# Kernel optimization log

Measured on AMD Instinct MI355X. Metric: run time of the kernel, lower is better.

## Reference

```python
import jax, jax.numpy as jnp
import numpy as np
import math

B, N, D = 16, 1024, 1024

def setup_inputs() -> dict:
    key = jax.random.key(0)
    k1, k2, k3, k4 = jax.random.split(key, 4)
    x = jax.random.normal(k1, (B, N, D), dtype=jnp.float32)
    # Keras 'random_normal' initializer defaults to stddev=0.05
    w_keys = jax.random.normal(k2, (N, N), dtype=jnp.float32) * 0.05
    w_queries = jax.random.normal(k3, (N, N), dtype=jnp.float32) * 0.05
    w_values = jax.random.normal(k4, (N, N), dtype=jnp.float32) * 0.05
    return {"x": x, "w_keys": w_keys, "w_queries": w_queries, "w_values": w_values}

def reference(x, w_keys, w_queries, w_values):
    # x: (B, N, D); weights: (N, N); fact = sqrt(N) per build(input_shape[1])
    fact = math.sqrt(x.shape[1])
    ip = jnp.swapaxes(x, 1, 2)              # (B, D, N)
    vk = ip @ w_keys                         # (B, D, N)
    vq = ip @ w_queries                      # (B, D, N)
    vv = ip @ w_values                       # (B, D, N)
    kq = jnp.einsum('bdn,ben->bde', vk, vq) / fact   # (B, D, D)
    sm = jax.nn.softmax(kq, axis=-1)         # softmax over last axis
    # tf: sm @ transpose(pm(vv)) == sm @ vv  since pm then transpose_b cancel
    out = jnp.einsum('bde,ben->bdn', sm, vv) # (B, D, N)
    return jnp.swapaxes(out, 1, 2)           # (B, N, D)
```

## Files before the change

kernel.cpp:

```cpp
#include <hip/hip_runtime.h>
#include <stdint.h>


typedef __bf16 bf16x8_t __attribute__((ext_vector_type(8)));
typedef float  f32x4_t  __attribute__((ext_vector_type(4)));

typedef __attribute__((address_space(3))) uint32_t as3_u32;
typedef __attribute__((address_space(1))) uint32_t as1_u32;

__device__ __forceinline__ void async_copy16(const void* g, const void* l) {
  __builtin_amdgcn_global_load_lds((const as1_u32*)(uintptr_t)g,
                                   (as3_u32*)(uint32_t)(uintptr_t)l,
                                   16, 0, 0);
}

__device__ __forceinline__ uint16_t f2bf(float f) {
  uint32_t x = __float_as_uint(f);
  return (uint16_t)((x + 0x7fffu + ((x >> 16) & 1u)) >> 16);
}
__device__ __forceinline__ float bf2f(uint16_t b) {
  return __uint_as_float(((uint32_t)b) << 16);
}

template <bool OUT_F32>
__global__ __launch_bounds__(512, 2)
void gemm_bt256(const uint16_t* __restrict__ A, const uint16_t* __restrict__ B,
                void* __restrict__ Cv, size_t sA, size_t sB, size_t sC,
                float alpha)
{
  __shared__ __align__(16) char smem[131072];

  const int lid  = blockIdx.x;
  const int xcd  = lid & 7;
  const int slot = lid >> 3;
  const int z    = (xcd << 1) | (slot >> 4);
  const int t16  = slot & 15;
  const int bm0  = (t16 >> 2) << 8;
  const int bn0  = (t16 & 3) << 8;

  A += (size_t)z * sA + ((size_t)bm0 << 10);
  B += (size_t)z * sB + ((size_t)bn0 << 10);

  const int t    = threadIdx.x;
  const int lane = t & 63;
  const int w    = t >> 6;
  const int q    = lane >> 4;
  const int r16  = lane & 15;
  const int wm   = (w >> 2) << 7;
  const int wn   = (w & 3) << 6;

  const int g0  = t >> 3;
  const int cp  = t & 7;
  const int ce  = (cp ^ (g0 & 7)) << 3;
  const int sAo = (g0 << 7) + (cp << 4);
  const int rB  = ((g0 >> 5) << 6) + (g0 & 31);
  const int sBo = (rB << 7) + (cp << 4);
  const uint16_t* Ab = A + ((size_t)g0 << 10) + ce;
  const uint16_t* Bb = B + ((size_t)rB << 10) + ce;

#define STAGE_A(s, kge, dst) do {                                              \
    async_copy16(Ab + (((s)*64 +   0) << 10) + (kge),                          \
                 smem + (dst) + sAo + (s)*8192);                               \
    async_copy16(Ab + (((s)*64 + 128) << 10) + (kge),                          \
                 smem + (dst) + sAo + (s)*8192 + 16384);                       \
  } while (0)
#define STAGE_B(s, kge, dst) do {                                              \
    async_copy16(Bb + (((s)*32 +   0) << 10) + (kge),                          \
                 smem + (dst) + 32768 + sBo + (s)*4096);                       \
    async_copy16(Bb + (((s)*32 + 128) << 10) + (kge),                          \
                 smem + (dst) + 32768 + sBo + (s)*4096 + 16384);               \
  } while (0)

  const int sl0 = ((0 + q) ^ (r16 & 7)) << 4;
  const int sl1 = ((4 + q) ^ (r16 & 7)) << 4;
  int aRd0 = ((wm + r16) << 7) + sl0;
  int aRd1 = ((wm + r16) << 7) + sl1;
  int bRd0 = 32768 + ((wn + r16) << 7) + sl0;
  int bRd1 = 32768 + ((wn + r16) << 7) + sl1;

  f32x4_t acc[8][4];
#pragma unroll
  for (int i = 0; i < 8; i++)
#pragma unroll
    for (int j = 0; j < 4; j++) acc[i][j] = (f32x4_t){0.f, 0.f, 0.f, 0.f};

  STAGE_A(0, 0, 0);
  STAGE_B(0, 0, 0);
  STAGE_B(1, 0, 0);
  STAGE_A(1, 0, 0);
  asm volatile("s_waitcnt vmcnt(4)" ::: "memory");
  __builtin_amdgcn_s_barrier();

  int nxt = 65536;
  for (int t0 = 0; t0 < 16; ++t0) {
    const int kge = ((t0 + 1) & 15) << 6;
    bf16x8_t af[4][2], bfA[2][2], bfB[2][2];

#pragma unroll
    for (int mi = 0; mi < 4; ++mi) {
      af[mi][0] = *(const bf16x8_t*)(smem + aRd0 + mi * 2048);
      af[mi][1] = *(const bf16x8_t*)(smem + aRd1 + mi * 2048);
    }
#pragma unroll
    for (int ni = 0; ni < 2; ++ni) {
      bfA[ni][0] = *(const bf16x8_t*)(smem + bRd0 + ni * 2048);
      bfA[ni][1] = *(const bf16x8_t*)(smem + bRd1 + ni * 2048);
    }
    STAGE_A(0, kge, nxt);
    asm volatile("s_waitcnt vmcnt(4)" ::: "memory");
    __builtin_amdgcn_s_barrier();
    asm volatile("s_waitcnt lgkmcnt(0)" ::: "memory");
    __builtin_amdgcn_sched_barrier(0);
    __builtin_amdgcn_s_setprio(1);
#pragma unroll
    for (int kk = 0; kk < 2; ++kk)
#pragma unroll
      for (int mi = 0; mi < 4; ++mi)
#pragma unroll
        for (int ni = 0; ni < 2; ++ni)
          acc[mi][ni] = __builtin_amdgcn_mfma_f32_16x16x32_bf16(
              af[mi][kk], bfA[ni][kk], acc[mi][ni], 0, 0, 0);
    __builtin_amdgcn_s_setprio(0);
    __builtin_amdgcn_s_barrier();

#pragma unroll
    for (int ni = 0; ni < 2; ++ni) {
      bfB[ni][0] = *(const bf16x8_t*)(smem + bRd0 + 4096 + ni * 2048);
      bfB[ni][1] = *(const bf16x8_t*)(smem + bRd1 + 4096 + ni * 2048);
    }
    STAGE_B(0, kge, nxt);
    asm volatile("s_waitcnt vmcnt(4)" ::: "memory");
    __builtin_amdgcn_s_barrier();
    asm volatile("s_waitcnt lgkmcnt(0)" ::: "memory");
    __builtin_amdgcn_sched_barrier(0);
    __builtin_amdgcn_s_setprio(1);
#pragma unroll
    for (int kk = 0; kk < 2; ++kk)
#pragma unroll
      for (int mi = 0; mi < 4; ++mi)
#pragma unroll
        for (int ni = 0; ni < 2; ++ni)
          acc[mi][2 + ni] = __builtin_amdgcn_mfma_f32_16x16x32_bf16(
              af[mi][kk], bfB[ni][kk], acc[mi][2 + ni], 0, 0, 0);
    __builtin_amdgcn_s_setprio(0);
    __builtin_amdgcn_s_barrier();

#pragma unroll
    for (int mi = 0; mi < 4; ++mi) {
      af[mi][0] = *(const bf16x8_t*)(smem + aRd0 + 8192 + mi * 2048);
      af[mi][1] = *(const bf16x8_t*)(smem + aRd1 + 8192 + mi * 2048);
    }
    STAGE_B(1, kge, nxt);
    __builtin_amdgcn_s_barrier();
    asm volatile("s_waitcnt lgkmcnt(0)" ::: "memory");
    __builtin_amdgcn_sched_barrier(0);
    __builtin_amdgcn_s_setprio(1);
#pragma unroll
    for (int kk = 0; kk < 2; ++kk)
#pragma unroll
      for (int mi = 0; mi < 4; ++mi)
#pragma unroll
        for (int ni = 0; ni < 2; ++ni)
          acc[4 + mi][2 + ni] = __builtin_amdgcn_mfma_f32_16x16x32_bf16(
              af[mi][kk], bfB[ni][kk], acc[4 + mi][2 + ni], 0, 0, 0);
    __builtin_amdgcn_s_setprio(0);
    __builtin_amdgcn_s_barrier();

    STAGE_A(1, kge, nxt);
    asm volatile("s_waitcnt vmcnt(4)" ::: "memory");
    __builtin_amdgcn_s_barrier();
    __builtin_amdgcn_s_setprio(1);
#pragma unroll
    for (int kk = 0; kk < 2; ++kk)
#pragma unroll
      for (int mi = 0; mi < 4; ++mi)
#pragma unroll
        for (int ni = 0; ni < 2; ++ni)
          acc[4 + mi][ni] = __builtin_amdgcn_mfma_f32_16x16x32_bf16(
              af[mi][kk], bfA[ni][kk], acc[4 + mi][ni], 0, 0, 0);
    __builtin_amdgcn_s_setprio(0);
    __builtin_amdgcn_s_barrier();

    aRd0 ^= 65536; aRd1 ^= 65536; bRd0 ^= 65536; bRd1 ^= 65536; nxt ^= 65536;
  }
#undef STAGE_A
#undef STAGE_B

  asm volatile("s_waitcnt vmcnt(0)" ::: "memory");
  __builtin_amdgcn_s_barrier();

  if (OUT_F32) {
    float* C = (float*)Cv + (size_t)z * sC;
#pragma unroll
    for (int mi = 0; mi < 8; ++mi)
#pragma unroll
      for (int ni = 0; ni < 4; ++ni)
#pragma unroll
        for (int r = 0; r < 4; ++r) {
          const int row = bm0 + wm + (mi << 4) + (q << 2) + r;
          const int col = bn0 + wn + (ni << 4) + r16;
          C[((size_t)row << 10) + col] = acc[mi][ni][r] * alpha;
        }
  } else {
    float* reg = (float*)smem + (size_t)w * 1056;
    uint16_t* C = (uint16_t*)Cv + (size_t)z * sC;
#pragma unroll
    for (int mi = 0; mi < 8; ++mi) {
#pragma unroll
      for (int ni = 0; ni < 4; ++ni)
#pragma unroll
        for (int r = 0; r < 4; ++r)
          reg[((q << 2) + r) * 66 + (ni << 4) + r16] = acc[mi][ni][r] * alpha;
#pragma unroll
      for (int it = 0; it < 8; ++it) {
        const int rr = (it << 1) + (lane >> 5);
        const int cc = (lane & 31) << 1;
        const float2 v = *(const float2*)(reg + rr * 66 + cc);
        const uint32_t p = (uint32_t)f2bf(v.x) | ((uint32_t)f2bf(v.y) << 16);
        const int row = bm0 + wm + (mi << 4) + rr;
        const int col = bn0 + wn + cc;
        *(uint32_t*)(C + ((size_t)row << 10) + col) = p;
      }
    }
  }
}

__global__ __launch_bounds__(256)
void transpose_cast(const float* __restrict__ src, uint16_t* __restrict__ dst,
                    int R, int Ccols, size_t sStride, size_t dStride)
{
  __shared__ float tile[32][33];
  const int z = blockIdx.z;
  src += (size_t)z * sStride;
  dst += (size_t)z * dStride;
  const int c0 = blockIdx.x << 5;
  const int r0 = blockIdx.y << 5;
  const int tx = threadIdx.x;
  const int ty = threadIdx.y;
#pragma unroll
  for (int i = 0; i < 32; i += 8)
    tile[ty + i][tx] = src[(size_t)(r0 + ty + i) * Ccols + (c0 + tx)];
  __syncthreads();
#pragma unroll
  for (int i = 0; i < 32; i += 8)
    dst[(size_t)(c0 + ty + i) * R + (r0 + tx)] = f2bf(tile[tx][ty + i]);
}

__global__ __launch_bounds__(256)
void transpose_cast_w(const float* __restrict__ w0, const float* __restrict__ w1,
                      const float* __restrict__ w2, uint16_t* __restrict__ o0,
                      uint16_t* __restrict__ o1, uint16_t* __restrict__ o2)
{
  __shared__ float tile[32][33];
  const int z = blockIdx.z;
  const float* src = (z == 0) ? w0 : (z == 1) ? w1 : w2;
  uint16_t* dst = (z == 0) ? o0 : (z == 1) ? o1 : o2;
  const int c0 = blockIdx.x << 5;
  const int r0 = blockIdx.y << 5;
  const int tx = threadIdx.x;
  const int ty = threadIdx.y;
#pragma unroll
  for (int i = 0; i < 32; i += 8)
    tile[ty + i][tx] = src[(size_t)(r0 + ty + i) * 1024 + (c0 + tx)];
  __syncthreads();
#pragma unroll
  for (int i = 0; i < 32; i += 8)
    dst[(size_t)(c0 + ty + i) * 1024 + (r0 + tx)] = f2bf(tile[tx][ty + i]);
}

__global__ __launch_bounds__(256)
void softmax_rows(const uint16_t* __restrict__ in, uint16_t* __restrict__ out)
{
  const size_t row = blockIdx.x;
  const ushort4* p4 = (const ushort4*)(in + row * 1024);
  ushort4* o4 = (ushort4*)(out + row * 1024);
  const int t = threadIdx.x;
  const int lane = t & 63;
  const int wv = t >> 6;

  const ushort4 u = p4[t];
  float v0 = bf2f(u.x), v1 = bf2f(u.y), v2 = bf2f(u.z), v3 = bf2f(u.w);

  float m = fmaxf(fmaxf(v0, v1), fmaxf(v2, v3));
#pragma unroll
  for (int s = 32; s; s >>= 1) m = fmaxf(m, __shfl_xor(m, s, 64));
  __shared__ float red[8];
  if (lane == 0) red[wv] = m;
  __syncthreads();
  m = fmaxf(fmaxf(red[0], red[1]), fmaxf(red[2], red[3]));

  const float e0 = __expf(v0 - m), e1 = __expf(v1 - m);
  const float e2 = __expf(v2 - m), e3 = __expf(v3 - m);
  float s = e0 + e1 + e2 + e3;
#pragma unroll
  for (int sh = 32; sh; sh >>= 1) s += __shfl_xor(s, sh, 64);
  if (lane == 0) red[4 + wv] = s;
  __syncthreads();
  s = red[4] + red[5] + red[6] + red[7];

  const float inv = 1.0f / s;
  ushort4 r;
  r.x = f2bf(e0 * inv); r.y = f2bf(e1 * inv);
  r.z = f2bf(e2 * inv); r.w = f2bf(e3 * inv);
  o4[t] = r;
}

extern "C" void kernel_launch(void* const* d_in, const int* in_sizes, int n_in,
                              void* d_out, int out_size, void* d_ws, size_t ws_size,
                              hipStream_t stream)
{
  const float* x  = (const float*)d_in[0];
  const float* wk = (const float*)d_in[1];
  const float* wq = (const float*)d_in[2];
  const float* wv = (const float*)d_in[3];
  float* out = (float*)d_out;

  constexpr int BB = 16, N = 1024, D = 1024;
  constexpr size_t DN = (size_t)D * N;

  char* ws = (char*)d_ws;
  uint16_t* xT  = (uint16_t*)(ws);
  uint16_t* Wtk = (uint16_t*)(ws + (32ull << 20));
  uint16_t* Wtq = (uint16_t*)(ws + (34ull << 20));
  uint16_t* Wtv = (uint16_t*)(ws + (36ull << 20));
  uint16_t* vk  = (uint16_t*)(ws + (38ull << 20));
  uint16_t* vq  = (uint16_t*)(ws + (70ull << 20));
  uint16_t* vvT = (uint16_t*)(ws + (102ull << 20));
  uint16_t* kq  = xT;
  uint16_t* sm  = vk;

  const dim3 tb(32, 8);
  transpose_cast<<<dim3(D / 32, N / 32, BB), tb, 0, stream>>>(x, xT, N, D, DN, DN);
  transpose_cast_w<<<dim3(N / 32, N / 32, 3), tb, 0, stream>>>(wk, wq, wv,
                                                               Wtk, Wtq, Wtv);

  gemm_bt256<false><<<256, 512, 0, stream>>>(xT, Wtk, vk, DN, 0, DN, 1.0f);
  gemm_bt256<false><<<256, 512, 0, stream>>>(xT, Wtq, vq, DN, 0, DN, 1.0f);
  gemm_bt256<false><<<256, 512, 0, stream>>>(Wtv, xT, vvT, 0, DN, DN, 1.0f);
  gemm_bt256<false><<<256, 512, 0, stream>>>(vk, vq, kq, DN, DN, DN, 0.03125f);
  softmax_rows<<<BB * D, 256, 0, stream>>>(kq, sm);
  gemm_bt256<true><<<256, 512, 0, stream>>>(vvT, sm, out, DN, DN, DN, 1.0f);
}
```

Before: 316.6 us.

## Precompute Wk·Wqᵀ product to replace two batched projections with one

Uses the identity kq = x^T Wk Wq^T x, computing the 1024x1024 weight product once with a split-K GEMM plus a reduction, instead of projecting x through Wk and Wq separately per batch. This removes one full batched GEMM over all 16 batches in exchange for a small extra GEMM and reduce. The main GEMM loop is also restructured so LDS fragment loads for the next stage are issued before the current MFMAs rather than waiting on lgkmcnt(0). Rounding the weight product to bf16 changes numerics slightly.

```diff
diff --git a/kernel.cpp b/kernel.cpp
--- a/kernel.cpp
+++ b/kernel.cpp
@@ -84,33 +84,37 @@
 #pragma unroll
     for (int j = 0; j < 4; j++) acc[i][j] = (f32x4_t){0.f, 0.f, 0.f, 0.f};
 
+  bf16x8_t afa[4][2], afb[4][2], bA[2][2], bB[2][2];
+
   STAGE_A(0, 0, 0);
   STAGE_B(0, 0, 0);
   STAGE_B(1, 0, 0);
   STAGE_A(1, 0, 0);
   asm volatile("s_waitcnt vmcnt(4)" ::: "memory");
   __builtin_amdgcn_s_barrier();
+#pragma unroll
+  for (int mi = 0; mi < 4; ++mi) {
+    afa[mi][0] = *(const bf16x8_t*)(smem + aRd0 + mi * 2048);
+    afa[mi][1] = *(const bf16x8_t*)(smem + aRd1 + mi * 2048);
+  }
+#pragma unroll
+  for (int ni = 0; ni < 2; ++ni) {
+    bA[ni][0] = *(const bf16x8_t*)(smem + bRd0 + ni * 2048);
+    bA[ni][1] = *(const bf16x8_t*)(smem + bRd1 + ni * 2048);
+  }
 
   int nxt = 65536;
   for (int t0 = 0; t0 < 16; ++t0) {
     const int kge = ((t0 + 1) & 15) << 6;
-    bf16x8_t af[4][2], bfA[2][2], bfB[2][2];
-
-#pragma unroll
-    for (int mi = 0; mi < 4; ++mi) {
-      af[mi][0] = *(const bf16x8_t*)(smem + aRd0 + mi * 2048);
-      af[mi][1] = *(const bf16x8_t*)(smem + aRd1 + mi * 2048);
-    }
-#pragma unroll
-    for (int ni = 0; ni < 2; ++ni) {
-      bfA[ni][0] = *(const bf16x8_t*)(smem + bRd0 + ni * 2048);
-      bfA[ni][1] = *(const bf16x8_t*)(smem + bRd1 + ni * 2048);
-    }
+
     STAGE_A(0, kge, nxt);
     asm volatile("s_waitcnt vmcnt(4)" ::: "memory");
     __builtin_amdgcn_s_barrier();
-    asm volatile("s_waitcnt lgkmcnt(0)" ::: "memory");
-    __builtin_amdgcn_sched_barrier(0);
+#pragma unroll
+    for (int ni = 0; ni < 2; ++ni) {
+      bB[ni][0] = *(const bf16x8_t*)(smem + bRd0 + 4096 + ni * 2048);
+      bB[ni][1] = *(const bf16x8_t*)(smem + bRd1 + 4096 + ni * 2048);
+    }
     __builtin_amdgcn_s_setprio(1);
 #pragma unroll
     for (int kk = 0; kk < 2; ++kk)
@@ -119,20 +123,18 @@
 #pragma unroll
         for (int ni = 0; ni < 2; ++ni)
           acc[mi][ni] = __builtin_amdgcn_mfma_f32_16x16x32_bf16(
-              af[mi][kk], bfA[ni][kk], acc[mi][ni], 0, 0, 0);
+              afa[mi][kk], bA[ni][kk], acc[mi][ni], 0, 0, 0);
     __builtin_amdgcn_s_setprio(0);
     __builtin_amdgcn_s_barrier();
 
-#pragma unroll
-    for (int ni = 0; ni < 2; ++ni) {
-      bfB[ni][0] = *(const bf16x8_t*)(smem + bRd0 + 4096 + ni * 2048);
-      bfB[ni][1] = *(const bf16x8_t*)(smem + bRd1 + 4096 + ni * 2048);
-    }
     STAGE_B(0, kge, nxt);
     asm volatile("s_waitcnt vmcnt(4)" ::: "memory");
     __builtin_amdgcn_s_barrier();
-    asm volatile("s_waitcnt lgkmcnt(0)" ::: "memory");
-    __builtin_amdgcn_sched_barrier(0);
+#pragma unroll
+    for (int mi = 0; mi < 4; ++mi) {
+      afb[mi][0] = *(const bf16x8_t*)(smem + aRd0 + 8192 + mi * 2048);
+      afb[mi][1] = *(const bf16x8_t*)(smem + aRd1 + 8192 + mi * 2048);
+    }
     __builtin_amdgcn_s_setprio(1);
 #pragma unroll
     for (int kk = 0; kk < 2; ++kk)
@@ -141,19 +143,12 @@
 #pragma unroll
         for (int ni = 0; ni < 2; ++ni)
           acc[mi][2 + ni] = __builtin_amdgcn_mfma_f32_16x16x32_bf16(
-              af[mi][kk], bfB[ni][kk], acc[mi][2 + ni], 0, 0, 0);
+              afa[mi][kk], bB[ni][kk], acc[mi][2 + ni], 0, 0, 0);
     __builtin_amdgcn_s_setprio(0);
     __builtin_amdgcn_s_barrier();
 
-#pragma unroll
-    for (int mi = 0; mi < 4; ++mi) {
-      af[mi][0] = *(const bf16x8_t*)(smem + aRd0 + 8192 + mi * 2048);
-      af[mi][1] = *(const bf16x8_t*)(smem + aRd1 + 8192 + mi * 2048);
-    }
     STAGE_B(1, kge, nxt);
     __builtin_amdgcn_s_barrier();
-    asm volatile("s_waitcnt lgkmcnt(0)" ::: "memory");
-    __builtin_amdgcn_sched_barrier(0);
     __builtin_amdgcn_s_setprio(1);
 #pragma unroll
     for (int kk = 0; kk < 2; ++kk)
@@ -162,7 +157,7 @@
 #pragma unroll
         for (int ni = 0; ni < 2; ++ni)
           acc[4 + mi][2 + ni] = __builtin_amdgcn_mfma_f32_16x16x32_bf16(
-              af[mi][kk], bfB[ni][kk], acc[4 + mi][2 + ni], 0, 0, 0);
+              afb[mi][kk], bB[ni][kk], acc[4 + mi][2 + ni], 0, 0, 0);
     __builtin_amdgcn_s_setprio(0);
     __builtin_amdgcn_s_barrier();
 
@@ -177,8 +172,18 @@
 #pragma unroll
         for (int ni = 0; ni < 2; ++ni)
           acc[4 + mi][ni] = __builtin_amdgcn_mfma_f32_16x16x32_bf16(
-              af[mi][kk], bfA[ni][kk], acc[4 + mi][ni], 0, 0, 0);
+              afb[mi][kk], bA[ni][kk], acc[4 + mi][ni], 0, 0, 0);
     __builtin_amdgcn_s_setprio(0);
+#pragma unroll
+    for (int mi = 0; mi < 4; ++mi) {
+      afa[mi][0] = *(const bf16x8_t*)(smem + (aRd0 ^ 65536) + mi * 2048);
+      afa[mi][1] = *(const bf16x8_t*)(smem + (aRd1 ^ 65536) + mi * 2048);
+    }
+#pragma unroll
+    for (int ni = 0; ni < 2; ++ni) {
+      bA[ni][0] = *(const bf16x8_t*)(smem + (bRd0 ^ 65536) + ni * 2048);
+      bA[ni][1] = *(const bf16x8_t*)(smem + (bRd1 ^ 65536) + ni * 2048);
+    }
     __builtin_amdgcn_s_barrier();
 
     aRd0 ^= 65536; aRd1 ^= 65536; bRd0 ^= 65536; bRd1 ^= 65536; nxt ^= 65536;
@@ -225,6 +230,128 @@
   }
 }
 
+__global__ __launch_bounds__(256, 4)
+void gemm128_splitk(const uint16_t* __restrict__ A, const uint16_t* __restrict__ B,
+                    float* __restrict__ P)
+{
+  __shared__ __align__(16) char smem[32768];
+  char* As = smem;
+  char* Bs = smem + 16384;
+
+  const int slice = blockIdx.x >> 6;
+  const int tile  = blockIdx.x & 63;
+  const int bm0   = (tile >> 3) << 7;
+  const int bn0   = (tile & 7) << 7;
+  const int koff  = slice << 8;
+
+  const int t    = threadIdx.x;
+  const int lane = t & 63;
+  const int w    = t >> 6;
+  const int q    = lane >> 4;
+  const int r16  = lane & 15;
+  const int wm   = (w >> 1) << 6;
+  const int wn   = (w & 1) << 6;
+
+  f32x4_t acc[4][4];
+#pragma unroll
+  for (int i = 0; i < 4; i++)
+#pragma unroll
+    for (int j = 0; j < 4; j++) acc[i][j] = (f32x4_t){0.f, 0.f, 0.f, 0.f};
+
+  for (int k0 = koff; k0 < koff + 256; k0 += 64) {
+#pragma unroll
+    for (int i = 0; i < 4; i++) {
+      const int o  = (i << 12) + (t << 4);
+      const int m  = o >> 7;
+      const int cp = (o >> 4) & 7;
+      const int c  = cp ^ (m & 7);
+      async_copy16(A + (size_t)(bm0 + m) * 1024 + (size_t)(k0 + (c << 3)), As + o);
+      async_copy16(B + (size_t)(bn0 + m) * 1024 + (size_t)(k0 + (c << 3)), Bs + o);
+    }
+    __syncthreads();
+#pragma unroll
+    for (int kk = 0; kk < 2; kk++) {
+      bf16x8_t af[4], bfr[4];
+#pragma unroll
+      for (int mi = 0; mi < 4; mi++) {
+        const int m = wm + (mi << 4) + r16;
+        const int c = (kk << 2) + q;
+        af[mi] = *(const bf16x8_t*)(As + (m << 7) + ((c ^ (m & 7)) << 4));
+      }
+#pragma unroll
+      for (int ni = 0; ni < 4; ni++) {
+        const int n = wn + (ni << 4) + r16;
+        const int c = (kk << 2) + q;
+        bfr[ni] = *(const bf16x8_t*)(Bs + (n << 7) + ((c ^ (n & 7)) << 4));
+      }
+#pragma unroll
+      for (int mi = 0; mi < 4; mi++)
+#pragma unroll
+        for (int ni = 0; ni < 4; ni++)
+          acc[mi][ni] = __builtin_amdgcn_mfma_f32_16x16x32_bf16(
+              af[mi], bfr[ni], acc[mi][ni], 0, 0, 0);
+    }
+    __syncthreads();
+  }
+
+  float* C = P + (size_t)slice * (1024u * 1024u);
+#pragma unroll
+  for (int mi = 0; mi < 4; mi++)
+#pragma unroll
+    for (int ni = 0; ni < 4; ni++)
+#pragma unroll
+      for (int r = 0; r < 4; r++) {
+        const int row = bm0 + wm + (mi << 4) + (q << 2) + r;
+        const int col = bn0 + wn + (ni << 4) + r16;
+        C[((size_t)row << 10) + col] = acc[mi][ni][r];
+      }
+}
+
+__global__ __launch_bounds__(256)
+void reduce_w2t(const float* __restrict__ P, uint16_t* __restrict__ W)
+{
+  const size_t i4 = (((size_t)blockIdx.x << 8) + threadIdx.x) << 2;
+  const float4 a = *(const float4*)(P + i4);
+  const float4 b = *(const float4*)(P + (1u << 20) + i4);
+  const float4 c = *(const float4*)(P + (2u << 20) + i4);
+  const float4 d = *(const float4*)(P + (3u << 20) + i4);
+  ushort4 r;
+  r.x = f2bf(a.x + b.x + c.x + d.x);
+  r.y = f2bf(a.y + b.y + c.y + d.y);
+  r.z = f2bf(a.z + b.z + c.z + d.z);
+  r.w = f2bf(a.w + b.w + c.w + d.w);
+  *(ushort4*)(W + i4) = r;
+}
+
+__global__ __launch_bounds__(256)
+void prep_w(const float* __restrict__ w0, const float* __restrict__ w1,
+            const float* __restrict__ w2, uint16_t* __restrict__ o0,
+            uint16_t* __restrict__ o1, uint16_t* __restrict__ o2)
+{
+  __shared__ float tile[32][33];
+  const int z = blockIdx.z;
+  const int c0 = blockIdx.x << 5;
+  const int r0 = blockIdx.y << 5;
+  const int tx = threadIdx.x;
+  const int ty = threadIdx.y;
+  if (z < 2) {
+    const float* src = z ? w1 : w0;
+    uint16_t* dst = z ? o1 : o0;
+#pragma unroll
+    for (int i = 0; i < 32; i += 8)
+      dst[(size_t)(r0 + ty + i) * 1024 + (c0 + tx)] =
+          f2bf(src[(size_t)(r0 + ty + i) * 1024 + (c0 + tx)]);
+  } else {
+#pragma unroll
+    for (int i = 0; i < 32; i += 8)
+      tile[ty + i][tx] = w2[(size_t)(r0 + ty + i) * 1024 + (c0 + tx)];
+    __syncthreads();
+#pragma unroll
+    for (int i = 0; i < 32; i += 8)
+      o2[(size_t)(c0 + ty + i) * 1024 + (r0 + tx)] = f2bf(tile[tx][ty + i]);
+  }
+}
+
 __global__ __launch_bounds__(256)
 void transpose_cast(const float* __restrict__ src, uint16_t* __restrict__ dst,
                     int R, int Ccols, size_t sStride, size_t dStride)
@@ -247,28 +374,6 @@
 }
 
 __global__ __launch_bounds__(256)
-void transpose_cast_w(const float* __restrict__ w0, const float* __restrict__ w1,
-                      const float* __restrict__ w2, uint16_t* __restrict__ o0,
-                      uint16_t* __restrict__ o1, uint16_t* __restrict__ o2)
-{
-  __shared__ float tile[32][33];
-  const int z = blockIdx.z;
-  const float* src = (z == 0) ? w0 : (z == 1) ? w1 : w2;
-  uint16_t* dst = (z == 0) ? o0 : (z == 1) ? o1 : o2;
-  const int c0 = blockIdx.x << 5;
-  const int r0 = blockIdx.y << 5;
-  const int tx = threadIdx.x;
-  const int ty = threadIdx.y;
-#pragma unroll
-  for (int i = 0; i < 32; i += 8)
-    tile[ty + i][tx] = src[(size_t)(r0 + ty + i) * 1024 + (c0 + tx)];
-  __syncthreads();
-#pragma unroll
-  for (int i = 0; i < 32; i += 8)
-    dst[(size_t)(c0 + ty + i) * 1024 + (r0 + tx)] = f2bf(tile[tx][ty + i]);
-}
-
-__global__ __launch_bounds__(256)
 void softmax_rows(const uint16_t* __restrict__ in, uint16_t* __restrict__ out)
 {
   const size_t row = blockIdx.x;
@@ -319,25 +424,25 @@
   constexpr size_t DN = (size_t)D * N;
 
   char* ws = (char*)d_ws;
-  uint16_t* xT  = (uint16_t*)(ws);
-  uint16_t* Wtk = (uint16_t*)(ws + (32ull << 20));
-  uint16_t* Wtq = (uint16_t*)(ws + (34ull << 20));
-  uint16_t* Wtv = (uint16_t*)(ws + (36ull << 20));
-  uint16_t* vk  = (uint16_t*)(ws + (38ull << 20));
-  uint16_t* vq  = (uint16_t*)(ws + (70ull << 20));
-  uint16_t* vvT = (uint16_t*)(ws + (102ull << 20));
-  uint16_t* kq  = xT;
-  uint16_t* sm  = vk;
+  uint16_t* xT   = (uint16_t*)(ws);
+  uint16_t* Wkc  = (uint16_t*)(ws + (32ull << 20));
+  uint16_t* Wqc  = (uint16_t*)(ws + (34ull << 20));
+  uint16_t* Wtv  = (uint16_t*)(ws + (36ull << 20));
+  uint16_t* W2Tc = (uint16_t*)(ws + (38ull << 20));
+  float*    W2p  = (float*)   (ws + (40ull << 20));
+  uint16_t* tmp  = (uint16_t*)(ws + (56ull << 20));
+  uint16_t* vvT  = (uint16_t*)(ws + (88ull << 20));
+  uint16_t* kq   = (uint16_t*)(ws + (120ull << 20));
+  uint16_t* sm   = tmp;
 
   const dim3 tb(32, 8);
+  prep_w<<<dim3(N / 32, N / 32, 3), tb, 0, stream>>>(wk, wq, wv, Wkc, Wqc, Wtv);
+  gemm128_splitk<<<256, 256, 0, stream>>>(Wqc, Wkc, W2p);
+  reduce_w2t<<<1024, 256, 0, stream>>>(W2p, W2Tc);
   transpose_cast<<<dim3(D / 32, N / 32, BB), tb, 0, stream>>>(x, xT, N, D, DN, DN);
-  transpose_cast_w<<<dim3(N / 32, N / 32, 3), tb, 0, stream>>>(wk, wq, wv,
-                                                               Wtk, Wtq, Wtv);
-
-  gemm_bt256<false><<<256, 512, 0, stream>>>(xT, Wtk, vk, DN, 0, DN, 1.0f);
-  gemm_bt256<false><<<256, 512, 0, stream>>>(xT, Wtq, vq, DN, 0, DN, 1.0f);
+  gemm_bt256<false><<<256, 512, 0, stream>>>(xT, W2Tc, tmp, DN, 0, DN, 1.0f);
   gemm_bt256<false><<<256, 512, 0, stream>>>(Wtv, xT, vvT, 0, DN, DN, 1.0f);
-  gemm_bt256<false><<<256, 512, 0, stream>>>(vk, vq, kq, DN, DN, DN, 0.03125f);
+  gemm_bt256<false><<<256, 512, 0, stream>>>(tmp, xT, kq, DN, DN, DN, 0.03125f);
   softmax_rows<<<BB * D, 256, 0, stream>>>(kq, sm);
   gemm_bt256<true><<<256, 512, 0, stream>>>(vvT, sm, out, DN, DN, DN, 1.0f);
 }
```

Measured after the change: 301.3 us. 4.8% less time.
